# Optimization experiments

Hardware: AMD Instinct MI355X
Metric: run time of the kernel (lower is better)

The kernel has to match this reference:

```python
import jax, jax.numpy as jnp
import numpy as np

# Config (matches init_kwargs)
IMG, PATCH, AC, PAD = 112, 8, 12, 2
DIM, HEADS, DH, DEPTH, MLP = 512, 8, 64, 12, 2048
INNER = HEADS * DH
PATCH_DIM = 3 * AC * AC
GRID = (IMG + 2 * PAD - AC) // PATCH + 1  # 14
N = GRID * GRID                            # 196 patches
EPS = 1e-5


def layer_norm(x, w, b, axis=-1):
    mu = x.mean(axis=axis, keepdims=True)
    var = ((x - mu) ** 2).mean(axis=axis, keepdims=True)
    return (x - mu) * jax.lax.rsqrt(var + EPS) * w + b


def setup_inputs() -> dict:
    key = jax.random.key(0)
    ks = jax.random.split(key, 24)
    g = lambda k, shp, s: (jax.random.normal(k, shp, jnp.float32) * s)
    d = {
        "img": g(ks[0], (32, 3, IMG, IMG), 1.0),
        "patch_w": g(ks[1], (PATCH_DIM, DIM), PATCH_DIM ** -0.5),
        "patch_b": jnp.zeros((DIM,), jnp.float32),
        "cls_token": g(ks[2], (1, 1, DIM), 1.0),
        "pos_emb": g(ks[3], (1, N + 1, DIM), 1.0),
        "ln1_w": jnp.ones((DEPTH, DIM)), "ln1_b": jnp.zeros((DEPTH, DIM)),
        "qkv_w": g(ks[4], (DEPTH, DIM, 3 * INNER), DIM ** -0.5),
        "reattn_w": g(ks[5], (DEPTH, HEADS, HEADS), 1.0),
        "reattn_ln_w": jnp.ones((DEPTH, HEADS)), "reattn_ln_b": jnp.zeros((DEPTH, HEADS)),
        "out_w": g(ks[6], (DEPTH, INNER, DIM), INNER ** -0.5),
        "out_b": jnp.zeros((DEPTH, DIM)),
        "ln2_w": jnp.ones((DEPTH, DIM)), "ln2_b": jnp.zeros((DEPTH, DIM)),
        "ff1_w": g(ks[7], (DEPTH, DIM, MLP), DIM ** -0.5), "ff1_b": jnp.zeros((DEPTH, MLP)),
        "ff2_w": g(ks[8], (DEPTH, MLP, DIM), MLP ** -0.5), "ff2_b": jnp.zeros((DEPTH, DIM)),
        "head_ln_w": jnp.ones((DIM,)), "head_ln_b": jnp.zeros((DIM,)),
    }
    return d


def _forward(img, patch_w, patch_b, cls_token, pos_emb, ln1_w, ln1_b, qkv_w,
             reattn_w, reattn_ln_w, reattn_ln_b, out_w, out_b, ln2_w, ln2_b,
             ff1_w, ff1_b, ff2_w, ff2_b, head_ln_w, head_ln_b):
    b = img.shape[0]
    scale = DH ** -0.5
    # Unfold: [B, C*AC*AC, GRID, GRID] with (c, kh, kw) channel ordering == torch.nn.Unfold
    patches = jax.lax.conv_general_dilated_patches(
        img, filter_shape=(AC, AC), window_strides=(PATCH, PATCH),
        padding=[(PAD, PAD), (PAD, PAD)])
    x = patches.reshape(b, PATCH_DIM, N).transpose(0, 2, 1)  # [b, n, patch_dim]
    x = x @ patch_w + patch_b                                 # [b, n, dim]
    cls = jnp.broadcast_to(cls_token, (b, 1, DIM))
    x = jnp.concatenate([cls, x], axis=1) + pos_emb[:, : N + 1]

    for l in range(DEPTH):
        # --- attention block (Residual(PreNorm(Attention))) ---
        h_in = layer_norm(x, ln1_w[l], ln1_b[l])
        qkv = h_in @ qkv_w[l]                                  # [b, n+1, 3*inner]
        q, k, v = jnp.split(qkv, 3, axis=-1)
        rs = lambda t: t.reshape(b, N + 1, HEADS, DH).transpose(0, 2, 1, 3)  # b h n d
        q, k, v = rs(q), rs(k), rs(v)
        dots = jnp.einsum('bhid,bhjd->bhij', q, k) * scale
        attn = jax.nn.softmax(dots, axis=-1)
        attn = jnp.einsum('bhij,hg->bgij', attn, reattn_w[l])  # re-attention head mix
        # LayerNorm over heads axis (axis=1)
        attn = layer_norm(attn, reattn_ln_w[l][None, :, None, None],
                          reattn_ln_b[l][None, :, None, None], axis=1)
        o = jnp.einsum('bhij,bhjd->bhid', attn, v)
        o = o.transpose(0, 2, 1, 3).reshape(b, N + 1, INNER)
        x = x + (o @ out_w[l] + out_b[l])
        # --- feedforward block ---
        h2 = layer_norm(x, ln2_w[l], ln2_b[l])
        h2 = jax.nn.gelu(h2 @ ff1_w[l] + ff1_b[l], approximate=False)
        x = x + (h2 @ ff2_w[l] + ff2_b[l])

    pooled = x[:, 0]                                           # cls pooling
    return layer_norm(pooled, head_ln_w, head_ln_b)


def reference(img, patch_w, patch_b, cls_token, pos_emb, ln1_w, ln1_b, qkv_w,
              reattn_w, reattn_ln_w, reattn_ln_b, out_w, out_b, ln2_w, ln2_b,
              ff1_w, ff1_b, ff2_w, ff2_b, head_ln_w, head_ln_b):
    return _forward(img, patch_w, patch_b, cls_token, pos_emb, ln1_w, ln1_b,
                    qkv_w, reattn_w, reattn_ln_w, reattn_ln_b, out_w, out_b,
                    ln2_w, ln2_b, ff1_w, ff1_b, ff2_w, ff2_b, head_ln_w, head_ln_b)
```

## Files before the change

kernel.cpp:

```cpp
#include <hip/hip_runtime.h>
#include <math.h>

#define SEQ    197
#define BATCH  32
#define ROWS   (BATCH * SEQ)
#define MPAD   6400
#define DIM    512
#define NHEADS 8
#define NDEPTH 12
#define MLPD   2048
#define PKD    448
#define SP     208
#define PSTR   224
#define VSTR   228
#define EPSF   1e-5f

typedef unsigned short ushort_t;
typedef __attribute__((ext_vector_type(8))) short  short8;
typedef __attribute__((ext_vector_type(4))) float  floatx4;

__device__ __forceinline__ float bf2f(ushort_t u) {
    union { unsigned int i; float f; } v; v.i = ((unsigned int)u) << 16; return v.f;
}
__device__ __forceinline__ ushort_t f2bf(float f) {
    union { float f; unsigned int i; } v; v.f = f;
    unsigned int r = v.i + 0x7fffu + ((v.i >> 16) & 1u);
    return (ushort_t)(r >> 16);
}
__device__ __forceinline__ void gl2lds16(const ushort_t* g, ushort_t* l) {
    __builtin_amdgcn_global_load_lds(
        (const __attribute__((address_space(1))) unsigned int*)g,
        (__attribute__((address_space(3))) unsigned int*)l, 16, 0, 0);
}
__device__ __forceinline__ float gelu_tanh(float v) {
    const float y = 0.7978845608028654f * fmaf(0.044715f * v, v * v, v);
    const float e = __expf(-2.f * fabsf(y));
    const float th = copysignf((1.f - e) * __builtin_amdgcn_rcpf(1.f + e), y);
    return 0.5f * v * (1.f + th);
}

__global__ __launch_bounds__(256) void wtrans_kernel(
    const float* __restrict__ W, ushort_t* __restrict__ Wt, int K, int N)
{
    const int l = blockIdx.z;
    W  += (size_t)l * K * N;
    Wt += (size_t)l * K * N;
    const int n0 = blockIdx.x * 32;
    const int k0 = blockIdx.y * 32;
    const int t = threadIdx.x;

    __shared__ float tile[32][33];
    {
        const int row = t >> 3;
        const int cq  = (t & 7) * 4;
        const float4 v = *(const float4*)(W + (size_t)(k0 + row) * N + n0 + cq);
        tile[row][cq + 0] = v.x;
        tile[row][cq + 1] = v.y;
        tile[row][cq + 2] = v.z;
        tile[row][cq + 3] = v.w;
    }
    __syncthreads();
    {
        const int n  = t >> 3;
        const int kq = (t & 7) * 4;
        ushort4 o;
        o.x = f2bf(tile[kq + 0][n]);
        o.y = f2bf(tile[kq + 1][n]);
        o.z = f2bf(tile[kq + 2][n]);
        o.w = f2bf(tile[kq + 3][n]);
        *(ushort4*)(Wt + (size_t)(n0 + n) * K + k0 + kq) = o;
    }
}

__global__ __launch_bounds__(256) void pwt_kernel(
    const float* __restrict__ pw, ushort_t* __restrict__ pwt)
{
    const int n = blockIdx.x;
    for (int k = threadIdx.x; k < PKD; k += 256)
        pwt[(size_t)n * PKD + k] = (k < 432) ? f2bf(pw[(size_t)k * DIM + n]) : (ushort_t)0;
}

__global__ __launch_bounds__(256) void im2col_kernel(
    const float* __restrict__ img, ushort_t* __restrict__ pcol)
{
    const int r = blockIdx.x;
    const int t = threadIdx.x;
    ushort_t* row = pcol + (size_t)r * PKD;
    const int b = r / SEQ;
    const int s = r - b * SEQ;
    const bool valid = (r < ROWS) && (s > 0);
    const int p = s - 1;
    const int gy = p / 14, gx = p - (p / 14) * 14;

    #pragma unroll
    for (int rep = 0; rep < 2; ++rep) {
        const int e = t + rep * 256;
        if (e >= PKD) break;
        float v = 0.f;
        if (valid && e < 432) {
            const int c = e / 144;
            const int rr = e - c * 144;
            const int fy = rr / 12, fx = rr - (rr / 12) * 12;
            const int py = gy * 8 - 2 + fy;
            const int px = gx * 8 - 2 + fx;
            if (py >= 0 && py < 112 && px >= 0 && px < 112)
                v = img[((size_t)(b * 3 + c) * 112 + py) * 112 + px];
        }
        row[e] = f2bf(v);
    }
}

__global__ __launch_bounds__(256) void pos_add_kernel(
    float* __restrict__ x, const float* __restrict__ cls, const float* __restrict__ pos)
{
    const int r = blockIdx.x;
    const int t = threadIdx.x;
    const int b = r / SEQ;
    const int s = r - b * SEQ;
    float* xr = x + (size_t)r * DIM;
    const float* pr = pos + (size_t)s * DIM;
    if (s == 0) {
        xr[t]       = cls[t]       + pr[t];
        xr[t + 256] = cls[t + 256] + pr[t + 256];
    } else {
        xr[t]       += pr[t];
        xr[t + 256] += pr[t + 256];
    }
}

__global__ __launch_bounds__(256) void ln4_kernel(
    const float* __restrict__ in, ushort_t* __restrict__ out,
    const float* __restrict__ g, const float* __restrict__ bta)
{
    const int t = threadIdx.x;
    const int w = t >> 6, lane = t & 63;
    const int r = blockIdx.x * 4 + w;
    const int off = lane * 8;
    const float* ip = in + (size_t)r * DIM + off;
    const float4 a = *(const float4*)ip;
    const float4 c = *(const float4*)(ip + 4);
    float s  = a.x + a.y + a.z + a.w + c.x + c.y + c.z + c.w;
    float ss = a.x*a.x + a.y*a.y + a.z*a.z + a.w*a.w + c.x*c.x + c.y*c.y + c.z*c.z + c.w*c.w;
    #pragma unroll
    for (int o = 32; o > 0; o >>= 1) {
        s  += __shfl_xor(s, o);
        ss += __shfl_xor(ss, o);
    }
    const float mu  = s * (1.f / 512.f);
    const float var = ss * (1.f / 512.f) - mu * mu;
    const float inv = rsqrtf(var + EPSF);
    const float4 g0 = *(const float4*)(g + off);
    const float4 g1 = *(const float4*)(g + off + 4);
    const float4 b0 = *(const float4*)(bta + off);
    const float4 b1 = *(const float4*)(bta + off + 4);
    ushort4 o0, o1;
    o0.x = f2bf((a.x - mu) * inv * g0.x + b0.x);
    o0.y = f2bf((a.y - mu) * inv * g0.y + b0.y);
    o0.z = f2bf((a.z - mu) * inv * g0.z + b0.z);
    o0.w = f2bf((a.w - mu) * inv * g0.w + b0.w);
    o1.x = f2bf((c.x - mu) * inv * g1.x + b1.x);
    o1.y = f2bf((c.y - mu) * inv * g1.y + b1.y);
    o1.z = f2bf((c.z - mu) * inv * g1.z + b1.z);
    o1.w = f2bf((c.w - mu) * inv * g1.w + b1.w);
    ushort_t* op = out + (size_t)r * DIM + off;
    *(ushort4*)op = o0;
    *(ushort4*)(op + 4) = o1;
}

__global__ __launch_bounds__(256) void ln_kernel(
    const float* __restrict__ in, float* __restrict__ out,
    const float* __restrict__ g, const float* __restrict__ bta,
    size_t in_stride, size_t out_stride)
{
    const int r = blockIdx.x;
    const int t = threadIdx.x;
    const float* ip = in + (size_t)r * in_stride;
    const float v0 = ip[t];
    const float v1 = ip[t + 256];
    float s = v0 + v1;
    float ss = v0 * v0 + v1 * v1;
    #pragma unroll
    for (int off = 32; off > 0; off >>= 1) {
        s  += __shfl_xor(s, off);
        ss += __shfl_xor(ss, off);
    }
    __shared__ float rs[4], rss[4];
    if ((t & 63) == 0) { rs[t >> 6] = s; rss[t >> 6] = ss; }
    __syncthreads();
    s  = rs[0] + rs[1] + rs[2] + rs[3];
    ss = rss[0] + rss[1] + rss[2] + rss[3];
    const float mu  = s * (1.f / 512.f);
    const float var = ss * (1.f / 512.f) - mu * mu;
    const float inv = rsqrtf(var + EPSF);
    float* op = out + (size_t)r * out_stride;
    op[t]       = (v0 - mu) * inv * g[t]       + bta[t];
    op[t + 256] = (v1 - mu) * inv * g[t + 256] + bta[t + 256];
}

template <int BM>
__global__ __launch_bounds__(256) void gemm_bf16_kernel(
    const ushort_t* __restrict__ A, const ushort_t* __restrict__ Bt,
    const float* __restrict__ bias, ushort_t* __restrict__ Cb,
    float* __restrict__ Cx, int N, int K, int mode)
{
    constexpr int RA = BM / 4;
    constexpr int MI = BM / 32;
    __shared__ ushort_t As[BM * 64];
    __shared__ ushort_t Bs[128 * 64];
    const int t = threadIdx.x;
    const int l = t & 63;
    const int w = t >> 6;
    const int bm = blockIdx.y * BM;
    const int bn = blockIdx.x * 128;
    const int wm = (w & 1) * (BM / 2);
    const int wn = (w >> 1) * 64;

    const int srow = l >> 3;
    const int skw  = ((l & 7) ^ srow) * 8;
    const ushort_t* gA = A  + (size_t)(bm + w * RA + srow) * K + skw;
    const ushort_t* gB = Bt + (size_t)(bn + w * 32 + srow) * K + skw;

    floatx4 acc[MI][4];
    #pragma unroll
    for (int i = 0; i < MI; ++i)
        #pragma unroll
        for (int j = 0; j < 4; ++j)
            acc[i][j] = (floatx4){0.f, 0.f, 0.f, 0.f};

    const int fr = l & 15;
    const int quad = l >> 4;
    const int c0 = ((quad ^ (fr & 7)) * 8);

    for (int k0 = 0; k0 < K; k0 += 64) {
        #pragma unroll
        for (int jc = 0; jc < RA / 8; ++jc)
            gl2lds16(gA + (size_t)(jc * 8) * K + k0, As + (w * RA + jc * 8) * 64);
        #pragma unroll
        for (int jc = 0; jc < 4; ++jc)
            gl2lds16(gB + (size_t)(jc * 8) * K + k0, Bs + (w * 32 + jc * 8) * 64);
        __syncthreads();
        #pragma unroll
        for (int half = 0; half < 2; ++half) {
            const int co = c0 ^ (half * 32);
            short8 af[MI], bf4[4];
            #pragma unroll
            for (int i = 0; i < MI; ++i)
                af[i] = *(const short8*)(As + (wm + i * 16 + fr) * 64 + co);
            #pragma unroll
            for (int j = 0; j < 4; ++j)
                bf4[j] = *(const short8*)(Bs + (wn + j * 16 + fr) * 64 + co);
            #pragma unroll
            for (int i = 0; i < MI; ++i)
                #pragma unroll
                for (int j = 0; j < 4; ++j)
                    acc[i][j] = __builtin_amdgcn_mfma_f32_16x16x32_bf16(
                        af[i], bf4[j], acc[i][j], 0, 0, 0);
        }
        __syncthreads();
    }

    float bv[4];
    #pragma unroll
    for (int j = 0; j < 4; ++j)
        bv[j] = bias ? bias[bn + wn + j * 16 + fr] : 0.f;

    const int r0 = quad * 4;
    #pragma unroll
    for (int i = 0; i < MI; ++i)
        #pragma unroll
        for (int r = 0; r < 4; ++r) {
            const size_t row = (size_t)(bm + wm + i * 16 + r0 + r);
            if (mode == 1) {
                float* cp = Cx + row * N + bn + wn + fr;
                #pragma unroll
                for (int j = 0; j < 4; ++j)
                    cp[j * 16] += acc[i][j][r] + bv[j];
            } else if (mode == 3) {
                float* cp = Cx + row * N + bn + wn + fr;
                #pragma unroll
                for (int j = 0; j < 4; ++j)
                    cp[j * 16] = acc[i][j][r] + bv[j];
            } else if (mode == 2) {
                ushort_t* cp = Cb + row * N + bn + wn + fr;
                #pragma unroll
                for (int j = 0; j < 4; ++j)
                    cp[j * 16] = f2bf(gelu_tanh(acc[i][j][r] + bv[j]));
            } else {
                ushort_t* cp = Cb + row * N + bn + wn + fr;
                #pragma unroll
                for (int j = 0; j < 4; ++j)
                    cp[j * 16] = f2bf(acc[i][j][r] + bv[j]);
            }
        }
}

__global__ __launch_bounds__(256) void qk_softmax_kernel(
    const ushort_t* __restrict__ qkv, float* __restrict__ P)
{
    const int bh = blockIdx.x;
    const int hf = blockIdx.y;
    const int b = bh >> 3, h = bh & 7;
    const int t = threadIdx.x;
    const int w = t >> 6, lane = t & 63;
    const int fr = lane & 15, quad = lane >> 4;
    const int cnt = hf ? 6 : 7;
    const int q0 = hf * 112;

    __shared__ ushort_t Qs[112 * 64];
    __shared__ ushort_t Ks[SP * 64];

    const size_t base = (size_t)(b * SEQ) * 1536;
    for (int e = t; e < SP * 16; e += 256) {
        const int r = e >> 4;
        const int d4 = (e & 15) * 4;
        *(ushort4*)(Ks + r * 64 + d4) =
            *(const ushort4*)(qkv + base + (size_t)r * 1536 + 512 + h * 64 + d4);
    }
    for (int e = t; e < 112 * 16; e += 256) {
        const int r = e >> 4;
        const int d4 = (e & 15) * 4;
        *(ushort4*)(Qs + r * 64 + d4) =
            *(const ushort4*)(qkv + base + (size_t)(q0 + r) * 1536 + h * 64 + d4);
    }
    __syncthreads();

    #pragma unroll
    for (int mi = 0; mi < 2; ++mi) {
        const int mfl = w * 2 + mi;
        if (mfl >= cnt) break;
        const int mf = hf * 7 + mfl;
        const short8 a0 = *(const short8*)(Qs + (mfl * 16 + fr) * 64 + quad * 8);
        const short8 a1 = *(const short8*)(Qs + (mfl * 16 + fr) * 64 + 32 + quad * 8);
        floatx4 acc[13];
        #pragma unroll
        for (int nf = 0; nf < 13; ++nf) {
            const short8 b0 = *(const short8*)(Ks + (nf * 16 + fr) * 64 + quad * 8);
            const short8 b1 = *(const short8*)(Ks + (nf * 16 + fr) * 64 + 32 + quad * 8);
            floatx4 z = (floatx4){0.f, 0.f, 0.f, 0.f};
            z = __builtin_amdgcn_mfma_f32_16x16x32_bf16(a0, b0, z, 0, 0, 0);
            acc[nf] = __builtin_amdgcn_mfma_f32_16x16x32_bf16(a1, b1, z, 0, 0, 0);
        }
        #pragma unroll
        for (int rr = 0; rr < 4; ++rr) {
            const bool maskc = (fr >= 5);
            float mx = -1e30f;
            #pragma unroll
            for (int nf = 0; nf < 13; ++nf) {
                const float v = (nf == 12 && maskc) ? -1e30f : acc[nf][rr] * 0.125f;
                mx = fmaxf(mx, v);
            }
            #pragma unroll
            for (int off = 1; off < 16; off <<= 1) mx = fmaxf(mx, __shfl_xor(mx, off));
            float sum = 0.f;
            #pragma unroll
            for (int nf = 0; nf < 13; ++nf) {
                const float v = (nf == 12 && maskc) ? -1e30f : acc[nf][rr] * 0.125f;
                const float pe = __expf(v - mx);
                acc[nf][rr] = pe;
                sum += pe;
            }
            #pragma unroll
            for (int off = 1; off < 16; off <<= 1) sum += __shfl_xor(sum, off);
            const float inv = 1.f / sum;
            const int i = mf * 16 + quad * 4 + rr;
            float* prow = P + ((size_t)bh * SP + i) * SP + fr;
            #pragma unroll
            for (int nf = 0; nf < 13; ++nf)
                prow[nf * 16] = acc[nf][rr] * inv;
        }
    }
}

__global__ __launch_bounds__(256) void mix_ln_kernel(
    const float* __restrict__ P, const float* __restrict__ rw,
    const float* __restrict__ lw, const float* __restrict__ lb,
    ushort_t* __restrict__ Pm)
{
    const int i = blockIdx.x;
    const int b = blockIdx.y;
    const int t = threadIdx.x;

    __shared__ float rws[64], lws[8], lbs[8];
    if (t < 64) rws[t] = rw[t];
    if (t < 8) { lws[t] = lw[t]; lbs[t] = lb[t]; }
    __syncthreads();

    float o[8];
    #pragma unroll
    for (int g = 0; g < 8; ++g) o[g] = 0.f;

    if (t < SEQ) {
        float a[8];
        #pragma unroll
        for (int h = 0; h < 8; ++h)
            a[h] = P[(((size_t)(b * 8 + h)) * SP + i) * SP + t];
        float m[8];
        float mu = 0.f;
        #pragma unroll
        for (int g = 0; g < 8; ++g) {
            float s = 0.f;
            #pragma unroll
            for (int h = 0; h < 8; ++h) s = fmaf(a[h], rws[h * 8 + g], s);
            m[g] = s;
            mu += s;
        }
        mu *= 0.125f;
        float var = 0.f;
        #pragma unroll
        for (int g = 0; g < 8; ++g) { const float d = m[g] - mu; var = fmaf(d, d, var); }
        var *= 0.125f;
        const float inv = rsqrtf(var + EPSF);
        #pragma unroll
        for (int g = 0; g < 8; ++g)
            o[g] = (m[g] - mu) * inv * lws[g] + lbs[g];
    }
    if (t < PSTR) {
        #pragma unroll
        for (int g = 0; g < 8; ++g)
            Pm[(((size_t)(b * 8 + g)) * SP + i) * PSTR + t] = f2bf(o[g]);
    }
}

__global__ __launch_bounds__(256) void av_kernel(
    const ushort_t* __restrict__ Pm, const ushort_t* __restrict__ qkv,
    ushort_t* __restrict__ o)
{
    const int bg = blockIdx.x;
    const int hf = blockIdx.y;
    const int b = bg >> 3, g = bg & 7;
    const int t = threadIdx.x;
    const int w = t >> 6, lane = t & 63;
    const int fr = lane & 15, quad = lane >> 4;
    const int cnt = hf ? 6 : 7;
    const int q0 = hf * 112;

    __shared__ ushort_t Vt[64 * VSTR];
    __shared__ ushort_t As[112 * 32];

    for (int e = t; e < 64 * VSTR / 4; e += 256)
        *(ushort4*)(Vt + e * 4) = (ushort4){0, 0, 0, 0};
    __syncthreads();

    const size_t vbase = (size_t)(b * SEQ) * 1536 + 1024 + g * 64;
    {
        const int d = t & 63;
        for (int j4 = (t >> 6) * 4; j4 < SEQ; j4 += 16) {
            ushort4 vv;
            vv.x = qkv[vbase + (size_t)(j4 + 0) * 1536 + d];
            vv.y = (j4 + 1 < SEQ) ? qkv[vbase + (size_t)(j4 + 1) * 1536 + d] : (ushort_t)0;
            vv.z = (j4 + 2 < SEQ) ? qkv[vbase + (size_t)(j4 + 2) * 1536 + d] : (ushort_t)0;
            vv.w = (j4 + 3 < SEQ) ? qkv[vbase + (size_t)(j4 + 3) * 1536 + d] : (ushort_t)0;
            *(ushort4*)(Vt + d * VSTR + j4) = vv;
        }
    }

    const ushort_t* gp = Pm + (size_t)bg * SP * PSTR + (size_t)q0 * PSTR;
    floatx4 acc[2][4];
    #pragma unroll
    for (int i = 0; i < 2; ++i)
        #pragma unroll
        for (int j = 0; j < 4; ++j)
            acc[i][j] = (floatx4){0.f, 0.f, 0.f, 0.f};

    for (int k0 = 0; k0 < PSTR; k0 += 32) {
        __syncthreads();
        #pragma unroll
        for (int rr = 0; rr < 2; ++rr) {
            const int row0 = (rr * 4 + w) * 16;
            if (row0 < cnt * 16)
                gl2lds16(gp + (size_t)(row0 + (lane >> 2)) * PSTR + k0 + (lane & 3) * 8,
                         As + row0 * 32);
        }
        __syncthreads();
        #pragma unroll
        for (int mi = 0; mi < 2; ++mi) {
            const int mfl = w + mi * 4;
            if (mfl >= cnt) break;
            const short8 af = *(const short8*)(As + (mfl * 16 + fr) * 32 + quad * 8);
            #pragma unroll
            for (int nf = 0; nf < 4; ++nf) {
                const short8 bfr = *(const short8*)(Vt + (nf * 16 + fr) * VSTR + k0 + quad * 8);
                acc[mi][nf] = __builtin_amdgcn_mfma_f32_16x16x32_bf16(af, bfr, acc[mi][nf], 0, 0, 0);
            }
        }
    }

    #pragma unroll
    for (int mi = 0; mi < 2; ++mi) {
        const int mfl = w + mi * 4;
        if (mfl >= cnt) break;
        #pragma unroll
        for (int rr = 0; rr < 4; ++rr) {
            const int i = (hf * 7 + mfl) * 16 + quad * 4 + rr;
            if (i < SEQ) {
                ushort_t* op = o + (size_t)(b * SEQ + i) * DIM + g * 64 + fr;
                #pragma unroll
                for (int nf = 0; nf < 4; ++nf)
                    op[nf * 16] = f2bf(acc[mi][nf][rr]);
            }
        }
    }
}

extern "C" void kernel_launch(void* const* d_in, const int* in_sizes, int n_in,
                              void* d_out, int out_size, void* d_ws, size_t ws_size,
                              hipStream_t stream)
{
    (void)in_sizes; (void)n_in; (void)out_size; (void)ws_size;

    const float* img       = (const float*)d_in[0];
    const float* patch_w   = (const float*)d_in[1];
    const float* patch_b   = (const float*)d_in[2];
    const float* cls_token = (const float*)d_in[3];
    const float* pos_emb   = (const float*)d_in[4];
    const float* ln1_w     = (const float*)d_in[5];
    const float* ln1_b     = (const float*)d_in[6];
    const float* qkv_w     = (const float*)d_in[7];
    const float* reattn_w  = (const float*)d_in[8];
    const float* reattn_lw = (const float*)d_in[9];
    const float* reattn_lb = (const float*)d_in[10];
    const float* out_w     = (const float*)d_in[11];
    const float* out_b     = (const float*)d_in[12];
    const float* ln2_w     = (const float*)d_in[13];
    const float* ln2_b     = (const float*)d_in[14];
    const float* ff1_w     = (const float*)d_in[15];
    const float* ff1_b     = (const float*)d_in[16];
    const float* ff2_w     = (const float*)d_in[17];
    const float* ff2_b     = (const float*)d_in[18];
    const float* head_lw   = (const float*)d_in[19];
    const float* head_lb   = (const float*)d_in[20];
    float* out = (float*)d_out;

    char* p = (char*)d_ws;
    float* x = (float*)p;            p += (size_t)MPAD * DIM * 4;
    ushort_t* hb = (ushort_t*)p;     p += (size_t)MPAD * DIM * 2;
    ushort_t* qkvb = (ushort_t*)p;   p += (size_t)MPAD * 1536 * 2;
    char* big = p;
    float* P = (float*)big;
    ushort_t* Pm = (ushort_t*)(big + (size_t)256 * SP * SP * 4);
    ushort_t* midb = (ushort_t*)big;
    p += (size_t)256 * SP * SP * 4 + (size_t)256 * SP * PSTR * 2;
    ushort_t* pcol = (ushort_t*)p;   p += (size_t)MPAD * PKD * 2;
    ushort_t* pwt  = (ushort_t*)p;   p += (size_t)DIM * PKD * 2;
    ushort_t* qkv_wt = (ushort_t*)p; p += (size_t)NDEPTH * 1536 * 512 * 2;
    ushort_t* out_wt = (ushort_t*)p; p += (size_t)NDEPTH * 512 * 512 * 2;
    ushort_t* ff1_wt = (ushort_t*)p; p += (size_t)NDEPTH * 2048 * 512 * 2;
    ushort_t* ff2_wt = (ushort_t*)p; p += (size_t)NDEPTH * 512 * 2048 * 2;

    wtrans_kernel<<<dim3(1536 / 32, 512 / 32, NDEPTH), 256, 0, stream>>>(qkv_w, qkv_wt, 512, 1536);
    wtrans_kernel<<<dim3(512 / 32, 512 / 32, NDEPTH), 256, 0, stream>>>(out_w, out_wt, 512, 512);
    wtrans_kernel<<<dim3(2048 / 32, 512 / 32, NDEPTH), 256, 0, stream>>>(ff1_w, ff1_wt, 512, 2048);
    wtrans_kernel<<<dim3(512 / 32, 2048 / 32, NDEPTH), 256, 0, stream>>>(ff2_w, ff2_wt, 2048, 512);
    pwt_kernel<<<DIM, 256, 0, stream>>>(patch_w, pwt);

    im2col_kernel<<<MPAD, 256, 0, stream>>>(img, pcol);
    gemm_bf16_kernel<64><<<dim3(DIM / 128, MPAD / 64), 256, 0, stream>>>(
        pcol, pwt, patch_b, nullptr, x, DIM, PKD, 3);
    pos_add_kernel<<<ROWS, 256, 0, stream>>>(x, cls_token, pos_emb);

    for (int l = 0; l < NDEPTH; ++l) {
        ln4_kernel<<<ROWS / 4, 256, 0, stream>>>(x, hb, ln1_w + l * DIM, ln1_b + l * DIM);
        gemm_bf16_kernel<128><<<dim3(1536 / 128, MPAD / 128), 256, 0, stream>>>(
            hb, qkv_wt + (size_t)l * 1536 * 512, nullptr, qkvb, nullptr, 1536, 512, 0);
        qk_softmax_kernel<<<dim3(BATCH * NHEADS, 2), 256, 0, stream>>>(qkvb, P);
        mix_ln_kernel<<<dim3(SEQ, BATCH), 256, 0, stream>>>(
            P, reattn_w + l * 64, reattn_lw + l * 8, reattn_lb + l * 8, Pm);
        av_kernel<<<dim3(BATCH * NHEADS, 2), 256, 0, stream>>>(Pm, qkvb, hb);
        gemm_bf16_kernel<64><<<dim3(DIM / 128, MPAD / 64), 256, 0, stream>>>(
            hb, out_wt + (size_t)l * 512 * 512, out_b + l * DIM, nullptr, x, DIM, 512, 1);
        ln4_kernel<<<ROWS / 4, 256, 0, stream>>>(x, hb, ln2_w + l * DIM, ln2_b + l * DIM);
        gemm_bf16_kernel<128><<<dim3(MLPD / 128, MPAD / 128), 256, 0, stream>>>(
            hb, ff1_wt + (size_t)l * 2048 * 512, ff1_b + l * MLPD, midb, nullptr, MLPD, 512, 2);
        gemm_bf16_kernel<64><<<dim3(DIM / 128, MPAD / 64), 256, 0, stream>>>(
            midb, ff2_wt + (size_t)l * 512 * 2048, ff2_b + l * DIM, nullptr, x, DIM, 2048, 1);
    }

    ln_kernel<<<BATCH, 256, 0, stream>>>(x, out, head_lw, head_lb, (size_t)SEQ * DIM, DIM);
}
```

Before: 2.142 ms.

## Fuse pos-add with first LN, template GEMM dims, swizzle K tile, batch mix_ln rows

New measurement: 2.028 ms. 1.06x faster.

```diff
diff --git a/kernel.cpp b/kernel.cpp
--- a/kernel.cpp
+++ b/kernel.cpp
@@ -13,6 +13,7 @@
 #define SP     208
 #define PSTR   224
 #define VSTR   228
+#define ASTR   40
 #define EPSF   1e-5f
 
 typedef unsigned short ushort_t;
@@ -110,8 +111,10 @@
     }
 }
 
-__global__ __launch_bounds__(256) void pos_add_kernel(
-    float* __restrict__ x, const float* __restrict__ cls, const float* __restrict__ pos)
+__global__ __launch_bounds__(256) void pos_add_ln_kernel(
+    float* __restrict__ x, const float* __restrict__ cls,
+    const float* __restrict__ pos, ushort_t* __restrict__ hb,
+    const float* __restrict__ g, const float* __restrict__ bta)
 {
     const int r = blockIdx.x;
     const int t = threadIdx.x;
@@ -119,13 +122,34 @@
     const int s = r - b * SEQ;
     float* xr = x + (size_t)r * DIM;
     const float* pr = pos + (size_t)s * DIM;
+    float v0, v1;
     if (s == 0) {
-        xr[t]       = cls[t]       + pr[t];
-        xr[t + 256] = cls[t + 256] + pr[t + 256];
+        v0 = cls[t]       + pr[t];
+        v1 = cls[t + 256] + pr[t + 256];
     } else {
-        xr[t]       += pr[t];
-        xr[t + 256] += pr[t + 256];
-    }
+        v0 = xr[t]       + pr[t];
+        v1 = xr[t + 256] + pr[t + 256];
+    }
+    xr[t] = v0;
+    xr[t + 256] = v1;
+    float sm = v0 + v1;
+    float ss = v0 * v0 + v1 * v1;
+    #pragma unroll
+    for (int off = 32; off > 0; off >>= 1) {
+        sm += __shfl_xor(sm, off);
+        ss += __shfl_xor(ss, off);
+    }
+    __shared__ float rs[4], rss[4];
+    if ((t & 63) == 0) { rs[t >> 6] = sm; rss[t >> 6] = ss; }
+    __syncthreads();
+    sm = rs[0] + rs[1] + rs[2] + rs[3];
+    ss = rss[0] + rss[1] + rss[2] + rss[3];
+    const float mu  = sm * (1.f / 512.f);
+    const float var = ss * (1.f / 512.f) - mu * mu;
+    const float inv = rsqrtf(var + EPSF);
+    ushort_t* op = hb + (size_t)r * DIM;
+    op[t]       = f2bf((v0 - mu) * inv * g[t]       + bta[t]);
+    op[t + 256] = f2bf((v1 - mu) * inv * g[t + 256] + bta[t + 256]);
 }
 
 __global__ __launch_bounds__(256) void ln4_kernel(
@@ -197,11 +221,11 @@
     op[t + 256] = (v1 - mu) * inv * g[t + 256] + bta[t + 256];
 }
 
-template <int BM>
+template <int BM, int NN, int KK, int MODE>
 __global__ __launch_bounds__(256) void gemm_bf16_kernel(
     const ushort_t* __restrict__ A, const ushort_t* __restrict__ Bt,
     const float* __restrict__ bias, ushort_t* __restrict__ Cb,
-    float* __restrict__ Cx, int N, int K, int mode)
+    float* __restrict__ Cx)
 {
     constexpr int RA = BM / 4;
     constexpr int MI = BM / 32;
@@ -217,8 +241,8 @@
 
     const int srow = l >> 3;
     const int skw  = ((l & 7) ^ srow) * 8;
-    const ushort_t* gA = A  + (size_t)(bm + w * RA + srow) * K + skw;
-    const ushort_t* gB = Bt + (size_t)(bn + w * 32 + srow) * K + skw;
+    const ushort_t* gA = A  + (size_t)(bm + w * RA + srow) * KK + skw;
+    const ushort_t* gB = Bt + (size_t)(bn + w * 32 + srow) * KK + skw;
 
     floatx4 acc[MI][4];
     #pragma unroll
@@ -231,13 +255,14 @@
     const int quad = l >> 4;
     const int c0 = ((quad ^ (fr & 7)) * 8);
 
-    for (int k0 = 0; k0 < K; k0 += 64) {
+    #pragma unroll 4
+    for (int k0 = 0; k0 < KK; k0 += 64) {
         #pragma unroll
         for (int jc = 0; jc < RA / 8; ++jc)
-            gl2lds16(gA + (size_t)(jc * 8) * K + k0, As + (w * RA + jc * 8) * 64);
+            gl2lds16(gA + (size_t)(jc * 8) * KK + k0, As + (w * RA + jc * 8) * 64);
         #pragma unroll
         for (int jc = 0; jc < 4; ++jc)
-            gl2lds16(gB + (size_t)(jc * 8) * K + k0, Bs + (w * 32 + jc * 8) * 64);
+            gl2lds16(gB + (size_t)(jc * 8) * KK + k0, Bs + (w * 32 + jc * 8) * 64);
         __syncthreads();
         #pragma unroll
         for (int half = 0; half < 2; ++half) {
@@ -270,23 +295,23 @@
         #pragma unroll
         for (int r = 0; r < 4; ++r) {
             const size_t row = (size_t)(bm + wm + i * 16 + r0 + r);
-            if (mode == 1) {
-                float* cp = Cx + row * N + bn + wn + fr;
+            if (MODE == 1) {
+                float* cp = Cx + row * NN + bn + wn + fr;
                 #pragma unroll
                 for (int j = 0; j < 4; ++j)
                     cp[j * 16] += acc[i][j][r] + bv[j];
-            } else if (mode == 3) {
-                float* cp = Cx + row * N + bn + wn + fr;
+            } else if (MODE == 3) {
+                float* cp = Cx + row * NN + bn + wn + fr;
                 #pragma unroll
                 for (int j = 0; j < 4; ++j)
                     cp[j * 16] = acc[i][j][r] + bv[j];
-            } else if (mode == 2) {
-                ushort_t* cp = Cb + row * N + bn + wn + fr;
+            } else if (MODE == 2) {
+                ushort_t* cp = Cb + row * NN + bn + wn + fr;
                 #pragma unroll
                 for (int j = 0; j < 4; ++j)
                     cp[j * 16] = f2bf(gelu_tanh(acc[i][j][r] + bv[j]));
             } else {
-                ushort_t* cp = Cb + row * N + bn + wn + fr;
+                ushort_t* cp = Cb + row * NN + bn + wn + fr;
                 #pragma unroll
                 for (int j = 0; j < 4; ++j)
                     cp[j * 16] = f2bf(acc[i][j][r] + bv[j]);
@@ -304,38 +329,35 @@
     const int w = t >> 6, lane = t & 63;
     const int fr = lane & 15, quad = lane >> 4;
     const int cnt = hf ? 6 : 7;
-    const int q0 = hf * 112;
-
-    __shared__ ushort_t Qs[112 * 64];
+
     __shared__ ushort_t Ks[SP * 64];
 
     const size_t base = (size_t)(b * SEQ) * 1536;
-    for (int e = t; e < SP * 16; e += 256) {
-        const int r = e >> 4;
-        const int d4 = (e & 15) * 4;
-        *(ushort4*)(Ks + r * 64 + d4) =
-            *(const ushort4*)(qkv + base + (size_t)r * 1536 + 512 + h * 64 + d4);
-    }
-    for (int e = t; e < 112 * 16; e += 256) {
-        const int r = e >> 4;
-        const int d4 = (e & 15) * 4;
-        *(ushort4*)(Qs + r * 64 + d4) =
-            *(const ushort4*)(qkv + base + (size_t)(q0 + r) * 1536 + h * 64 + d4);
+    for (int e = t; e < SP * 8; e += 256) {
+        const int r = e >> 3;
+        const int c = e & 7;
+        *(short8*)(Ks + r * 64 + ((c ^ (r & 7)) * 8)) =
+            *(const short8*)(qkv + base + (size_t)r * 1536 + 512 + h * 64 + c * 8);
     }
     __syncthreads();
+
+    const int cx0 = (quad ^ (fr & 7)) * 8;
+    const int cx1 = ((quad + 4) ^ (fr & 7)) * 8;
 
     #pragma unroll
     for (int mi = 0; mi < 2; ++mi) {
         const int mfl = w * 2 + mi;
         if (mfl >= cnt) break;
         const int mf = hf * 7 + mfl;
-        const short8 a0 = *(const short8*)(Qs + (mfl * 16 + fr) * 64 + quad * 8);
-        const short8 a1 = *(const short8*)(Qs + (mfl * 16 + fr) * 64 + 32 + quad * 8);
+        const size_t qrow = base + (size_t)(mf * 16 + fr) * 1536 + h * 64;
+        const short8 a0 = *(const short8*)(qkv + qrow + quad * 8);
+        const short8 a1 = *(const short8*)(qkv + qrow + 32 + quad * 8);
         floatx4 acc[13];
         #pragma unroll
         for (int nf = 0; nf < 13; ++nf) {
-            const short8 b0 = *(const short8*)(Ks + (nf * 16 + fr) * 64 + quad * 8);
-            const short8 b1 = *(const short8*)(Ks + (nf * 16 + fr) * 64 + 32 + quad * 8);
+            const ushort_t* kr = Ks + (nf * 16 + fr) * 64;
+            const short8 b0 = *(const short8*)(kr + cx0);
+            const short8 b1 = *(const short8*)(kr + cx1);
             floatx4 z = (floatx4){0.f, 0.f, 0.f, 0.f};
             z = __builtin_amdgcn_mfma_f32_16x16x32_bf16(a0, b0, z, 0, 0, 0);
             acc[nf] = __builtin_amdgcn_mfma_f32_16x16x32_bf16(a1, b1, z, 0, 0, 0);
@@ -376,7 +398,6 @@
     const float* __restrict__ lw, const float* __restrict__ lb,
     ushort_t* __restrict__ Pm)
 {
-    const int i = blockIdx.x;
     const int b = blockIdx.y;
     const int t = threadIdx.x;
 
@@ -385,39 +406,43 @@
     if (t < 8) { lws[t] = lw[t]; lbs[t] = lb[t]; }
     __syncthreads();
 
-    float o[8];
-    #pragma unroll
-    for (int g = 0; g < 8; ++g) o[g] = 0.f;
-
-    if (t < SEQ) {
-        float a[8];
-        #pragma unroll
-        for (int h = 0; h < 8; ++h)
-            a[h] = P[(((size_t)(b * 8 + h)) * SP + i) * SP + t];
-        float m[8];
-        float mu = 0.f;
-        #pragma unroll
-        for (int g = 0; g < 8; ++g) {
-            float s = 0.f;
-            #pragma unroll
-            for (int h = 0; h < 8; ++h) s = fmaf(a[h], rws[h * 8 + g], s);
-            m[g] = s;
-            mu += s;
-        }
-        mu *= 0.125f;
-        float var = 0.f;
-        #pragma unroll
-        for (int g = 0; g < 8; ++g) { const float d = m[g] - mu; var = fmaf(d, d, var); }
-        var *= 0.125f;
-        const float inv = rsqrtf(var + EPSF);
-        #pragma unroll
-        for (int g = 0; g < 8; ++g)
-            o[g] = (m[g] - mu) * inv * lws[g] + lbs[g];
-    }
-    if (t < PSTR) {
-        #pragma unroll
-        for (int g = 0; g < 8; ++g)
-            Pm[(((size_t)(b * 8 + g)) * SP + i) * PSTR + t] = f2bf(o[g]);
+    for (int ii = 0; ii < 4; ++ii) {
+        const int i = blockIdx.x * 4 + ii;
+        if (i >= SEQ) break;
+        float o[8];
+        #pragma unroll
+        for (int g = 0; g < 8; ++g) o[g] = 0.f;
+
+        if (t < SEQ) {
+            float a[8];
+            #pragma unroll
+            for (int h = 0; h < 8; ++h)
+                a[h] = P[(((size_t)(b * 8 + h)) * SP + i) * SP + t];
+            float m[8];
+            float mu = 0.f;
+            #pragma unroll
+            for (int g = 0; g < 8; ++g) {
+                float s = 0.f;
+                #pragma unroll
+                for (int h = 0; h < 8; ++h) s = fmaf(a[h], rws[h * 8 + g], s);
+                m[g] = s;
+                mu += s;
+            }
+            mu *= 0.125f;
+            float var = 0.f;
+            #pragma unroll
+            for (int g = 0; g < 8; ++g) { const float d = m[g] - mu; var = fmaf(d, d, var); }
+            var *= 0.125f;
+            const float inv = rsqrtf(var + EPSF);
+            #pragma unroll
+            for (int g = 0; g < 8; ++g)
+                o[g] = (m[g] - mu) * inv * lws[g] + lbs[g];
+        }
+        if (t < PSTR) {
+            #pragma unroll
+            for (int g = 0; g < 8; ++g)
+                Pm[(((size_t)(b * 8 + g)) * SP + i) * PSTR + t] = f2bf(o[g]);
+        }
     }
 }
 
@@ -435,7 +460,7 @@
     const int q0 = hf * 112;
 
     __shared__ ushort_t Vt[64 * VSTR];
-    __shared__ ushort_t As[112 * 32];
+    __shared__ ushort_t As[112 * ASTR];
 
     for (int e = t; e < 64 * VSTR / 4; e += 256)
         *(ushort4*)(Vt + e * 4) = (ushort4){0, 0, 0, 0};
@@ -462,21 +487,26 @@
         for (int j = 0; j < 4; ++j)
             acc[i][j] = (floatx4){0.f, 0.f, 0.f, 0.f};
 
+    const int nrows = cnt * 16;
+
     for (int k0 = 0; k0 < PSTR; k0 += 32) {
         __syncthreads();
         #pragma unroll
-        for (int rr = 0; rr < 2; ++rr) {
-            const int row0 = (rr * 4 + w) * 16;
-            if (row0 < cnt * 16)
-                gl2lds16(gp + (size_t)(row0 + (lane >> 2)) * PSTR + k0 + (lane & 3) * 8,
-                         As + row0 * 32);
+        for (int rep = 0; rep < 2; ++rep) {
+            const int e = t + rep * 256;
+            const int r = e >> 2;
+            const int c = e & 3;
+            if (r < nrows) {
+                const short8 v = *(const short8*)(gp + (size_t)r * PSTR + k0 + c * 8);
+                *(short8*)(As + r * ASTR + c * 8) = v;
+            }
         }
         __syncthreads();
         #pragma unroll
         for (int mi = 0; mi < 2; ++mi) {
             const int mfl = w + mi * 4;
             if (mfl >= cnt) break;
-            const short8 af = *(const short8*)(As + (mfl * 16 + fr) * 32 + quad * 8);
+            const short8 af = *(const short8*)(As + (mfl * 16 + fr) * ASTR + quad * 8);
             #pragma unroll
             for (int nf = 0; nf < 4; ++nf) {
                 const short8 bfr = *(const short8*)(Vt + (nf * 16 + fr) * VSTR + k0 + quad * 8);
@@ -554,25 +584,26 @@
     pwt_kernel<<<DIM, 256, 0, stream>>>(patch_w, pwt);
 
     im2col_kernel<<<MPAD, 256, 0, stream>>>(img, pcol);
-    gemm_bf16_kernel<64><<<dim3(DIM / 128, MPAD / 64), 256, 0, stream>>>(
-        pcol, pwt, patch_b, nullptr, x, DIM, PKD, 3);
-    pos_add_kernel<<<ROWS, 256, 0, stream>>>(x, cls_token, pos_emb);
+    gemm_bf16_kernel<64, 512, PKD, 3><<<dim3(DIM / 128, MPAD / 64), 256, 0, stream>>>(
+        pcol, pwt, patch_b, nullptr, x);
+    pos_add_ln_kernel<<<ROWS, 256, 0, stream>>>(x, cls_token, pos_emb, hb, ln1_w, ln1_b);
 
     for (int l = 0; l < NDEPTH; ++l) {
-        ln4_kernel<<<ROWS / 4, 256, 0, stream>>>(x, hb, ln1_w + l * DIM, ln1_b + l * DIM);
-        gemm_bf16_kernel<128><<<dim3(1536 / 128, MPAD / 128), 256, 0, stream>>>(
-            hb, qkv_wt + (size_t)l * 1536 * 512, nullptr, qkvb, nullptr, 1536, 512, 0);
+        if (l > 0)
+            ln4_kernel<<<ROWS / 4, 256, 0, stream>>>(x, hb, ln1_w + l * DIM, ln1_b + l * DIM);
+        gemm_bf16_kernel<128, 1536, 512, 0><<<dim3(1536 / 128, MPAD / 128), 256, 0, stream>>>(
+            hb, qkv_wt + (size_t)l * 1536 * 512, nullptr, qkvb, nullptr);
         qk_softmax_kernel<<<dim3(BATCH * NHEADS, 2), 256, 0, stream>>>(qkvb, P);
-        mix_ln_kernel<<<dim3(SEQ, BATCH), 256, 0, stream>>>(
+        mix_ln_kernel<<<dim3(50, BATCH), 256, 0, stream>>>(
             P, reattn_w + l * 64, reattn_lw + l * 8, reattn_lb + l * 8, Pm);
         av_kernel<<<dim3(BATCH * NHEADS, 2), 256, 0, stream>>>(Pm, qkvb, hb);
-        gemm_bf16_kernel<64><<<dim3(DIM / 128, MPAD / 64), 256, 0, stream>>>(
-            hb, out_wt + (size_t)l * 512 * 512, out_b + l * DIM, nullptr, x, DIM, 512, 1);
+        gemm_bf16_kernel<64, 512, 512, 1><<<dim3(DIM / 128, MPAD / 64), 256, 0, stream>>>(
+            hb, out_wt + (size_t)l * 512 * 512, out_b + l * DIM, nullptr, x);
         ln4_kernel<<<ROWS / 4, 256, 0, stream>>>(x, hb, ln2_w + l * DIM, ln2_b + l * DIM);
-        gemm_bf16_kernel<128><<<dim3(MLPD / 128, MPAD / 128), 256, 0, stream>>>(
-            hb, ff1_wt + (size_t)l * 2048 * 512, ff1_b + l * MLPD, midb, nullptr, MLPD, 512, 2);
-        gemm_bf16_kernel<64><<<dim3(DIM / 128, MPAD / 64), 256, 0, stream>>>(
-            midb, ff2_wt + (size_t)l * 512 * 2048, ff2_b + l * DIM, nullptr, x, DIM, 2048, 1);
+        gemm_bf16_kernel<128, 2048, 512, 2><<<dim3(MLPD / 128, MPAD / 128), 256, 0, stream>>>(
+            hb, ff1_wt + (size_t)l * 2048 * 512, ff1_b + l * MLPD, midb, nullptr);
+        gemm_bf16_kernel<64, 512, 2048, 1><<<dim3(DIM / 128, MPAD / 64), 256, 0, stream>>>(
+            midb, ff2_wt + (size_t)l * 512 * 2048, ff2_b + l * DIM, nullptr, x);
     }
 
     ln_kernel<<<BATCH, 256, 0, stream>>>(x, out, head_lw, head_lb, (size_t)SEQ * DIM, DIM);
```
